# Performance work log

Hardware: AMD Instinct MI355X
Metric: run time of the kernel (lower is better)

## Reference

```python
import jax, jax.numpy as jnp
import numpy as np

N_SPK = 2048   # number of speakers
U = 32         # utterances per speaker (half enrollment, half test)
D = 256        # embedding dim
EPS = 1e-8     # F.cosine_similarity eps (norm clamp)


def setup_inputs() -> dict:
    key = jax.random.key(0)
    k1, = jax.random.split(key, 1)
    embeddings = jax.random.normal(k1, (N_SPK * U, D), dtype=jnp.float32)
    labels = jnp.repeat(jnp.arange(N_SPK, dtype=jnp.int64), U)
    alpha = jnp.float32(10.0)
    beta = jnp.float32(-5.0)
    return {"embeddings": embeddings, "labels": labels, "alpha": alpha, "beta": beta}


def _ge2e_loss(embeddings, labels_np, alpha, beta):
    # labels_np: host numpy int labels (constant). Balanced: each speaker has U utts.
    n_spk = int(labels_np.max()) + 1
    u = labels_np.shape[0] // n_spk
    order = np.argsort(labels_np, kind="stable")  # group by speaker, preserve order
    emb = embeddings[order].reshape(n_spk, u, -1)           # [N, U, D]
    half = u // 2
    enroll, test = emb[:, :half], emb[:, half:]             # [N, U/2, D]
    cent = enroll.mean(axis=1)                              # [N, D]
    tn = test / jnp.maximum(jnp.linalg.norm(test, axis=-1, keepdims=True), EPS)
    cn = cent / jnp.maximum(jnp.linalg.norm(cent, axis=-1, keepdims=True), EPS)
    # cosine sim of every test utt (speaker m, utt t) vs every centroid n
    sims = alpha * jnp.einsum("mtd,nd->mtn", tn, cn) + beta  # [N, U/2, N]
    e = jnp.exp(sims)
    total = e.sum(axis=(0, 1))                               # [N] sum over all test utts per centroid
    idx = jnp.arange(n_spk)
    pos_sum = e[idx, :, idx].sum(axis=1)                     # [N] own-speaker test utts
    neg_sum = total - pos_sum                                # sum over other speakers' test utts
    loss = jnp.mean(jnp.log(neg_sum) - jnp.log(pos_sum))
    return loss


def reference(embeddings, labels, alpha, beta):
    labels_np = np.asarray(labels)
    return _ge2e_loss(embeddings, labels_np, alpha, beta)
```

## Files before the change

### kernel.cpp

```cpp
#include <hip/hip_runtime.h>
#include <hip/hip_bf16.h>
#include <stdint.h>

#define N_SPK 2048
#define UU 32
#define DD 256
#define HALF_U 16
#define M_ROWS (N_SPK * HALF_U)

#define BM 128
#define BN 128
#define BK 64

typedef __attribute__((ext_vector_type(8))) short short8;
typedef __attribute__((ext_vector_type(4))) float f32x4;

typedef const __attribute__((address_space(1))) void ga_void;
typedef __attribute__((address_space(3))) void ls_void;

__device__ __forceinline__ void gld16(const void* g, void* l) {
    __builtin_amdgcn_global_load_lds((ga_void*)(uintptr_t)g,
                                     (ls_void*)(uintptr_t)l, 16, 0, 0);
}

__device__ __forceinline__ unsigned short f2bf(float x) {
    union { float f; unsigned u; } c; c.f = x;
    unsigned r = c.u + 0x7fffu + ((c.u >> 16) & 1u);
    return (unsigned short)(r >> 16);
}

__global__ __launch_bounds__(256) void prep_kernel(const float* __restrict__ emb,
                                                   unsigned short* __restrict__ tn,
                                                   unsigned short* __restrict__ cn,
                                                   float* __restrict__ zbuf)
{
    if (blockIdx.x == 0) {
        #pragma unroll
        for (int i = 0; i < 16; ++i) zbuf[threadIdx.x + 256 * i] = 0.0f;
    }

    const int w = threadIdx.x >> 6;
    const int l = threadIdx.x & 63;
    const int task = blockIdx.x * 4 + w;

    float4 v;
    if (task < M_ROWS) {
        const int m = task >> 4;
        const int t = task & 15;
        const size_t grow = (size_t)m * UU + HALF_U + t;
        v = *(const float4*)(emb + grow * DD + 4 * l);
    } else {
        const int n = task - M_ROWS;
        float ax = 0.f, ay = 0.f, az = 0.f, aw = 0.f;
        const float* base = emb + (size_t)n * UU * DD + 4 * l;
        #pragma unroll
        for (int j = 0; j < HALF_U; ++j) {
            float4 e = *(const float4*)(base + j * DD);
            ax += e.x; ay += e.y; az += e.z; aw += e.w;
        }
        const float inv = 1.0f / 16.0f;
        v = make_float4(ax * inv, ay * inv, az * inv, aw * inv);
    }
    float ss = v.x * v.x + v.y * v.y + v.z * v.z + v.w * v.w;
    #pragma unroll
    for (int d = 1; d < 64; d <<= 1) ss += __shfl_xor(ss, d);
    const float sc = 1.0f / fmaxf(sqrtf(ss), 1e-8f);

    ushort4 o;
    o.x = f2bf(v.x * sc); o.y = f2bf(v.y * sc);
    o.z = f2bf(v.z * sc); o.w = f2bf(v.w * sc);
    unsigned short* dst = (task < M_ROWS)
        ? (tn + (size_t)task * DD + 4 * l)
        : (cn + (size_t)(task - M_ROWS) * DD + 4 * l);
    *(ushort4*)dst = o;
}

__global__ __launch_bounds__(256, 3) void gemm_kernel(const unsigned short* __restrict__ tnb,
                                                      const unsigned short* __restrict__ cnb,
                                                      const float* __restrict__ alphaP,
                                                      const float* __restrict__ betaP,
                                                      float* __restrict__ total,
                                                      float* __restrict__ pos)
{
    __shared__ __align__(16) char As[BM * BK * 2];
    __shared__ __align__(16) char Bs[BN * BK * 2];
    __shared__ float csum[BN];

    const int tid = threadIdx.x;
    const int l = tid & 63;
    const int w = tid >> 6;
    const int wr = w >> 1, wc = w & 1;
    const int r16 = l & 15, hi = l >> 4;

    const int bid = blockIdx.x;
    const int tile = (bid & 7) * 512 + (bid >> 3);
    const int bm = tile >> 4;
    const int bn = tile & 15;

    const char* gA = (const char*)tnb + (size_t)bm * BM * 512;
    const char* gB = (const char*)cnb + (size_t)bn * BN * 512;

    f32x4 acc[4][4] = {};

    for (int kt = 0; kt < 4; ++kt) {
        #pragma unroll
        for (int i = 0; i < 4; ++i) {
            const int off = i * 4096 + tid * 16;
            const int row = off >> 7;
            const int sc  = ((off >> 4) & 7) ^ (row & 7);
            const int goff = row * 512 + kt * 128 + sc * 16;
            gld16(gA + goff, As + off);
            gld16(gB + goff, Bs + off);
        }
        __syncthreads();

        #pragma unroll
        for (int kk = 0; kk < 2; ++kk) {
            short8 a[4], b[4];
            #pragma unroll
            for (int ni = 0; ni < 4; ++ni) {
                const int row = wc * 64 + ni * 16 + r16;
                const int c16 = (kk * 4 + hi) ^ (row & 7);
                b[ni] = *(const short8*)(Bs + row * 128 + c16 * 16);
            }
            #pragma unroll
            for (int mi = 0; mi < 4; ++mi) {
                const int row = wr * 64 + mi * 16 + r16;
                const int c16 = (kk * 4 + hi) ^ (row & 7);
                a[mi] = *(const short8*)(As + row * 128 + c16 * 16);
            }
            #pragma unroll
            for (int mi = 0; mi < 4; ++mi)
                #pragma unroll
                for (int ni = 0; ni < 4; ++ni)
                    acc[mi][ni] = __builtin_amdgcn_mfma_f32_16x16x32_bf16(
                        a[mi], b[ni], acc[mi][ni], 0, 0, 0);
        }
        __syncthreads();
    }

    const float alpha = *alphaP;
    const float beta  = *betaP;
    const bool diag = ((bm >> 4) == bn);

    if (tid < BN) csum[tid] = 0.0f;
    __syncthreads();

    #pragma unroll
    for (int ni = 0; ni < 4; ++ni) {
        const int colg = bn * BN + wc * 64 + ni * 16 + r16;
        float cs = 0.f;
        #pragma unroll
        for (int mi = 0; mi < 4; ++mi) {
            const int rowbase = bm * BM + wr * 64 + mi * 16 + hi * 4;
            #pragma unroll
            for (int r = 0; r < 4; ++r) {
                const float e = __expf(alpha * acc[mi][ni][r] + beta);
                cs += e;
                if (diag && ((rowbase + r) >> 4) == colg)
                    atomicAdd(pos + colg, e);
            }
        }
        cs += __shfl_xor(cs, 16);
        cs += __shfl_xor(cs, 32);
        if (hi == 0) atomicAdd(&csum[wc * 64 + ni * 16 + r16], cs);
    }
    __syncthreads();
    if (tid < BN) atomicAdd(total + bn * BN + tid, csum[tid]);
}

__global__ __launch_bounds__(256) void finalize_kernel(const float* __restrict__ total,
                                                       const float* __restrict__ pos,
                                                       float* __restrict__ out)
{
    const int tid = threadIdx.x;
    float s = 0.f;
    for (int i = tid; i < N_SPK; i += 256) {
        const float p = pos[i];
        const float t = total[i];
        s += logf(t - p) - logf(p);
    }
    #pragma unroll
    for (int d = 1; d < 64; d <<= 1) s += __shfl_xor(s, d);
    __shared__ float wsum[4];
    if ((tid & 63) == 0) wsum[tid >> 6] = s;
    __syncthreads();
    if (tid == 0) out[0] = (wsum[0] + wsum[1] + wsum[2] + wsum[3]) * (1.0f / (float)N_SPK);
}

extern "C" void kernel_launch(void* const* d_in, const int* in_sizes, int n_in,
                              void* d_out, int out_size, void* d_ws, size_t ws_size,
                              hipStream_t stream)
{
    const float* emb    = (const float*)d_in[0];
    const float* alphaP = (const float*)d_in[2];
    const float* betaP  = (const float*)d_in[3];
    float* out = (float*)d_out;

    char* ws = (char*)d_ws;
    unsigned short* tn = (unsigned short*)ws;
    unsigned short* cn = (unsigned short*)(ws + 16777216);
    float* total       = (float*)(ws + 16777216 + 1048576);
    float* pos         = total + N_SPK;

    hipLaunchKernelGGL(prep_kernel, dim3((M_ROWS + N_SPK) / 4), dim3(256), 0, stream,
                       emb, tn, cn, total );
    hipLaunchKernelGGL(gemm_kernel, dim3(M_ROWS / BM * (N_SPK / BN)), dim3(256), 0, stream,
                       tn, cn, alphaP, betaP, total, pos);
    hipLaunchKernelGGL(finalize_kernel, dim3(1), dim3(256), 0, stream,
                       total, pos, out);
}
```

Before: 153.7 us.

## Quantize normalized embeddings to FP8 and load MFMA operands directly from global

The prep kernel now writes normalized test and centroid vectors as FP8 (E4M3) instead of bf16, permuting bytes within each row so each lane's MFMA operand is one contiguous 16-byte load. The GEMM drops LDS staging and barriers, reads operands straight from global/L2 into registers, uses the fp8 MFMA, and raises the occupancy hint. This halves operand bytes and doubles MFMA throughput, but FP8 precision on cosine similarities scaled by alpha=10 before exp may push the loss past tolerance. Skipping LDS also means each block refetches overlapping rows from cache.

```diff
diff --git a/kernel.cpp b/kernel.cpp
--- a/kernel.cpp
+++ b/kernel.cpp
@@ -8,30 +8,12 @@
 #define HALF_U 16
 #define M_ROWS (N_SPK * HALF_U)
 
-#define BM 128
-#define BN 128
-#define BK 64
-
-typedef __attribute__((ext_vector_type(8))) short short8;
 typedef __attribute__((ext_vector_type(4))) float f32x4;
-
-typedef const __attribute__((address_space(1))) void ga_void;
-typedef __attribute__((address_space(3))) void ls_void;
-
-__device__ __forceinline__ void gld16(const void* g, void* l) {
-    __builtin_amdgcn_global_load_lds((ga_void*)(uintptr_t)g,
-                                     (ls_void*)(uintptr_t)l, 16, 0, 0);
-}
-
-__device__ __forceinline__ unsigned short f2bf(float x) {
-    union { float f; unsigned u; } c; c.f = x;
-    unsigned r = c.u + 0x7fffu + ((c.u >> 16) & 1u);
-    return (unsigned short)(r >> 16);
-}
+typedef __attribute__((ext_vector_type(2))) long long2_t;
 
 __global__ __launch_bounds__(256) void prep_kernel(const float* __restrict__ emb,
-                                                   unsigned short* __restrict__ tn,
-                                                   unsigned short* __restrict__ cn,
+                                                   uint8_t* __restrict__ tn8,
+                                                   uint8_t* __restrict__ cn8,
                                                    float* __restrict__ zbuf)
 {
     if (blockIdx.x == 0) {
@@ -66,25 +48,29 @@
     for (int d = 1; d < 64; d <<= 1) ss += __shfl_xor(ss, d);
     const float sc = 1.0f / fmaxf(sqrtf(ss), 1e-8f);
 
-    ushort4 o;
-    o.x = f2bf(v.x * sc); o.y = f2bf(v.y * sc);
-    o.z = f2bf(v.z * sc); o.w = f2bf(v.w * sc);
-    unsigned short* dst = (task < M_ROWS)
-        ? (tn + (size_t)task * DD + 4 * l)
-        : (cn + (size_t)(task - M_ROWS) * DD + 4 * l);
-    *(ushort4*)dst = o;
+    int p = __builtin_amdgcn_cvt_pk_fp8_f32(v.x * sc, v.y * sc, 0, 0);
+    p     = __builtin_amdgcn_cvt_pk_fp8_f32(v.z * sc, v.w * sc, p, 1);
+
+    const int d0  = 4 * l;
+    const int t4  = d0 >> 6;
+    const int hi4 = (d0 >> 3) & 3;
+    const int hf  = (d0 >> 5) & 1;
+    const int pos = t4 * 64 + hi4 * 16 + hf * 8 + (d0 & 7);
+
+    uint8_t* dst = (task < M_ROWS)
+        ? (tn8 + (size_t)task * DD + pos)
+        : (cn8 + (size_t)(task - M_ROWS) * DD + pos);
+    *(int*)dst = p;
 }
 
-__global__ __launch_bounds__(256, 3) void gemm_kernel(const unsigned short* __restrict__ tnb,
-                                                      const unsigned short* __restrict__ cnb,
+__global__ __launch_bounds__(256, 4) void gemm_kernel(const uint8_t* __restrict__ tn8,
+                                                      const uint8_t* __restrict__ cn8,
                                                       const float* __restrict__ alphaP,
                                                       const float* __restrict__ betaP,
                                                       float* __restrict__ total,
                                                       float* __restrict__ pos)
 {
-    __shared__ __align__(16) char As[BM * BK * 2];
-    __shared__ __align__(16) char Bs[BN * BK * 2];
-    __shared__ float csum[BN];
+    __shared__ float csum[128];
 
     const int tid = threadIdx.x;
     const int l = tid & 63;
@@ -97,62 +83,48 @@
     const int bm = tile >> 4;
     const int bn = tile & 15;
 
-    const char* gA = (const char*)tnb + (size_t)bm * BM * 512;
-    const char* gB = (const char*)cnb + (size_t)bn * BN * 512;
+    const uint8_t* Abase = tn8 + (size_t)(bm * 128 + wr * 64 + r16) * DD + hi * 16;
+    const uint8_t* Bbase = cn8 + (size_t)(bn * 128 + wc * 64 + r16) * DD + hi * 16;
 
     f32x4 acc[4][4] = {};
 
-    for (int kt = 0; kt < 4; ++kt) {
+    #pragma unroll
+    for (int t = 0; t < 4; ++t) {
+        long2_t a2[4], b2[4];
         #pragma unroll
-        for (int i = 0; i < 4; ++i) {
-            const int off = i * 4096 + tid * 16;
-            const int row = off >> 7;
-            const int sc  = ((off >> 4) & 7) ^ (row & 7);
-            const int goff = row * 512 + kt * 128 + sc * 16;
-            gld16(gA + goff, As + off);
-            gld16(gB + goff, Bs + off);
-        }
-        __syncthreads();
-
+        for (int mi = 0; mi < 4; ++mi)
+            a2[mi] = *(const long2_t*)(Abase + (size_t)mi * 16 * DD + t * 64);
         #pragma unroll
-        for (int kk = 0; kk < 2; ++kk) {
-            short8 a[4], b[4];
+        for (int ni = 0; ni < 4; ++ni)
+            b2[ni] = *(const long2_t*)(Bbase + (size_t)ni * 16 * DD + t * 64);
+        #pragma unroll
+        for (int mi = 0; mi < 4; ++mi)
             #pragma unroll
-            for (int ni = 0; ni < 4; ++ni) {
-                const int row = wc * 64 + ni * 16 + r16;
-                const int c16 = (kk * 4 + hi) ^ (row & 7);
-                b[ni] = *(const short8*)(Bs + row * 128 + c16 * 16);
-            }
+            for (int ni = 0; ni < 4; ++ni)
+                acc[mi][ni] = __builtin_amdgcn_mfma_f32_16x16x32_fp8_fp8(
+                    a2[mi][0], b2[ni][0], acc[mi][ni], 0, 0, 0);
+        #pragma unroll
+        for (int mi = 0; mi < 4; ++mi)
             #pragma unroll
-            for (int mi = 0; mi < 4; ++mi) {
-                const int row = wr * 64 + mi * 16 + r16;
-                const int c16 = (kk * 4 + hi) ^ (row & 7);
-                a[mi] = *(const short8*)(As + row * 128 + c16 * 16);
-            }
-            #pragma unroll
-            for (int mi = 0; mi < 4; ++mi)
-                #pragma unroll
-                for (int ni = 0; ni < 4; ++ni)
-                    acc[mi][ni] = __builtin_amdgcn_mfma_f32_16x16x32_bf16(
-                        a[mi], b[ni], acc[mi][ni], 0, 0, 0);
-        }
-        __syncthreads();
+            for (int ni = 0; ni < 4; ++ni)
+                acc[mi][ni] = __builtin_amdgcn_mfma_f32_16x16x32_fp8_fp8(
+                    a2[mi][1], b2[ni][1], acc[mi][ni], 0, 0, 0);
     }
 
     const float alpha = *alphaP;
     const float beta  = *betaP;
     const bool diag = ((bm >> 4) == bn);
 
-    if (tid < BN) csum[tid] = 0.0f;
+    if (tid < 128) csum[tid] = 0.0f;
     __syncthreads();
 
     #pragma unroll
     for (int ni = 0; ni < 4; ++ni) {
-        const int colg = bn * BN + wc * 64 + ni * 16 + r16;
+        const int colg = bn * 128 + wc * 64 + ni * 16 + r16;
         float cs = 0.f;
         #pragma unroll
         for (int mi = 0; mi < 4; ++mi) {
-            const int rowbase = bm * BM + wr * 64 + mi * 16 + hi * 4;
+            const int rowbase = bm * 128 + wr * 64 + mi * 16 + hi * 4;
             #pragma unroll
             for (int r = 0; r < 4; ++r) {
                 const float e = __expf(alpha * acc[mi][ni][r] + beta);
@@ -166,7 +138,7 @@
         if (hi == 0) atomicAdd(&csum[wc * 64 + ni * 16 + r16], cs);
     }
     __syncthreads();
-    if (tid < BN) atomicAdd(total + bn * BN + tid, csum[tid]);
+    if (tid < 128) atomicAdd(total + bn * 128 + tid, csum[tid]);
 }
 
 __global__ __launch_bounds__(256) void finalize_kernel(const float* __restrict__ total,
@@ -198,15 +170,15 @@
     float* out = (float*)d_out;
 
     char* ws = (char*)d_ws;
-    unsigned short* tn = (unsigned short*)ws;
-    unsigned short* cn = (unsigned short*)(ws + 16777216);
-    float* total       = (float*)(ws + 16777216 + 1048576);
-    float* pos         = total + N_SPK;
+    uint8_t* tn8 = (uint8_t*)ws;
+    uint8_t* cn8 = (uint8_t*)(ws + 8388608);
+    float* total = (float*)(ws + 8388608 + 524288);
+    float* pos   = total + N_SPK;
 
     hipLaunchKernelGGL(prep_kernel, dim3((M_ROWS + N_SPK) / 4), dim3(256), 0, stream,
-                       emb, tn, cn, total );
-    hipLaunchKernelGGL(gemm_kernel, dim3(M_ROWS / BM * (N_SPK / BN)), dim3(256), 0, stream,
-                       tn, cn, alphaP, betaP, total, pos);
+                       emb, tn8, cn8, total );
+    hipLaunchKernelGGL(gemm_kernel, dim3(M_ROWS / 128 * (N_SPK / 128)), dim3(256), 0, stream,
+                       tn8, cn8, alphaP, betaP, total, pos);
     hipLaunchKernelGGL(finalize_kernel, dim3(1), dim3(256), 0, stream,
                        total, pos, out);
 }
```

New measurement: 176.8 us. 1.15x slower.
